# Kernel tuning notes

Hardware: AMD Instinct MI355X
Metric: run time of the kernel (lower is better)

## Reference

```python
import jax, jax.numpy as jnp
from jax import lax
import numpy as np

B, T, C_IN, H, W = 2, 4, 128, 64, 64
D_MODEL, N_Q, N_POINTS, PATCH, N_LAYERS = 256, 300, 8, 3, 6


def _sine_pos(Hh, Ww, d, temperature=10000.0):
    # mask is all-False, so cumsum of ones -> arange(1..H)/H * 2pi
    two_pi = 2.0 * np.pi
    yn = (jnp.arange(1, Hh + 1, dtype=jnp.float32) / (Hh + 1e-6)) * two_pi
    xn = (jnp.arange(1, Ww + 1, dtype=jnp.float32) / (Ww + 1e-6)) * two_pi
    q = d // 4
    i = jnp.arange(q, dtype=jnp.float32)
    dim_t = temperature ** (2.0 * jnp.floor(i / 2.0) / q)
    py = yn[:, None] / dim_t
    px = xn[:, None] / dim_t
    py = jnp.stack([jnp.sin(py), jnp.cos(py)], axis=-1).reshape(Hh, 2 * q)
    px = jnp.stack([jnp.sin(px), jnp.cos(px)], axis=-1).reshape(Ww, 2 * q)
    pos = jnp.concatenate([
        jnp.broadcast_to(py[:, None, :], (Hh, Ww, 2 * q)),
        jnp.broadcast_to(px[None, :, :], (Hh, Ww, 2 * q)),
    ], axis=-1)
    return jnp.transpose(pos, (2, 0, 1))  # [d,H,W]


def _sample_scale(fmap, ref, ps):
    # fmap [B,C,h,w]; ref [B,nQ,nP,2] in [0,1]. Bilinear grid_sample,
    # padding_mode='border', align_corners=True -> direct gather (no replication).
    Bc, C, h, w = fmap.shape
    half = (ps - 1) / 2.0
    off = jnp.linspace(-half, half, ps, dtype=jnp.float32)
    oy, ox = jnp.meshgrid(off, off, indexing='ij')  # [ps,ps]
    gx = ref[..., 0, None, None] * 2.0 - 1.0 + ox * (2.0 / w)  # [B,nQ,nP,ps,ps]
    gy = ref[..., 1, None, None] * 2.0 - 1.0 + oy * (2.0 / h)
    x = jnp.clip((gx + 1.0) * 0.5 * (w - 1), 0.0, w - 1.0)
    y = jnp.clip((gy + 1.0) * 0.5 * (h - 1), 0.0, h - 1.0)
    x0 = jnp.floor(x); y0 = jnp.floor(y)
    wx = x - x0; wy = y - y0
    x0i = x0.astype(jnp.int32); y0i = y0.astype(jnp.int32)
    x1i = jnp.minimum(x0i + 1, w - 1); y1i = jnp.minimum(y0i + 1, h - 1)

    def per_b(fb, y0b, x0b, y1b, x1b, wxb, wyb):
        v00 = fb[:, y0b, x0b]  # [C,nQ,nP,ps,ps]
        v01 = fb[:, y0b, x1b]
        v10 = fb[:, y1b, x0b]
        v11 = fb[:, y1b, x1b]
        return (v00 * (1 - wxb) * (1 - wyb) + v01 * wxb * (1 - wyb)
                + v10 * (1 - wxb) * wyb + v11 * wxb * wyb)

    out = jax.vmap(per_b)(fmap, y0i, x0i, y1i, x1i, wx, wy)  # [B,C,nQ,nP,ps,ps]
    return jnp.transpose(out, (0, 2, 3, 4, 5, 1))  # [B,nQ,nP,ps,ps,C]


def reference(feat, pred_boxes_init, w_tf, b_tf, w_in, b_in, w_lat, b_lat, w_sm, b_sm,
              q_embed, q_pos, Wq, bq, Wo, bo, Wp1, bp1, Wp2, bp2,
              w_r1, b_r1, w_r2, b_r2, w_b1, b_b1, w_b2, b_b2, w_cls, b_cls):
    Bb, Tt, Cin, Hh, Ww = feat.shape
    d = w_in.shape[0]
    nP = w_r2.shape[0] // 2
    ps = int(round((Wp1.shape[-1] // d) ** 0.5))
    # temporal fuse: Conv3d kernel (3,1,1), padding (1,0,0)
    x = lax.conv_general_dilated(jnp.transpose(feat, (0, 2, 1, 3, 4)), w_tf,
                                 (1, 1, 1), [(1, 1), (0, 0), (0, 0)],
                                 dimension_numbers=('NCDHW', 'OIDHW', 'NCDHW'))
    x = x + b_tf[None, :, None, None, None]
    x = x.mean(axis=2)  # [B,Cin,H,W]
    x = jnp.einsum('bchw,dc->bdhw', x, w_in) + b_in[None, :, None, None]
    x = x + _sine_pos(Hh, Ww, d)[None]
    # FPN over scales {1,2,4}: avg_pool -> 1x1 lateral -> 3x3 smooth
    feats = []
    for i, s in enumerate((1, 2, 4)):
        xi = x if s == 1 else x.reshape(Bb, d, Hh // s, s, Ww // s, s).mean(axis=(3, 5))
        xi = jnp.einsum('bchw,oc->bohw', xi, w_lat[i]) + b_lat[i][None, :, None, None]
        xi = lax.conv_general_dilated(xi, w_sm[i], (1, 1), [(1, 1), (1, 1)],
                                      dimension_numbers=('NCHW', 'OIHW', 'NCHW'))
        xi = xi + b_sm[i][None, :, None, None]
        feats.append(xi)
    nQ = q_embed.shape[0]
    queries = jnp.broadcast_to((q_embed + q_pos)[None], (Bb, nQ, d))
    boxes = pred_boxes_init
    inv_sqrt_d = 1.0 / float(np.sqrt(d))
    for l in range(Wq.shape[0]):
        h1 = jax.nn.relu(jnp.einsum('bqd,od->bqo', queries, w_r1) + b_r1)
        ro = jnp.tanh(jnp.einsum('bqd,od->bqo', h1, w_r2) + b_r2)
        ro = ro.reshape(Bb, nQ, nP, 2) * 0.5
        ref = jnp.clip(boxes[:, :, None, :2] + ro, 0.0, 1.0)
        sampled = jnp.concatenate([_sample_scale(f, ref, ps) for f in feats], axis=2)
        sampled = sampled[:, :, :nP]  # truncate multi-scale concat back to nP
        flat = sampled.reshape(Bb, nQ, nP, ps * ps * d)
        pv = jax.nn.relu(jnp.einsum('bqpi,oi->bqpo', flat, Wp1[l]) + bp1[l])
        pv = jnp.einsum('bqpd,od->bqpo', pv, Wp2[l]) + bp2[l]
        kv = pv.mean(axis=2)  # [B,nP_q,d] -> [B,nQ,d]
        q = jnp.einsum('bqd,od->bqo', queries, Wq[l]) + bq[l]
        attn = jax.nn.softmax(jnp.einsum('bqd,bkd->bqk', q, kv) * inv_sqrt_d, axis=-1)
        out = jnp.einsum('bqk,bkd->bqd', attn, kv)
        queries = queries + (jnp.einsum('bqd,od->bqo', out, Wo[l]) + bo[l])
        hb = jax.nn.relu(jnp.einsum('bqd,od->bqo', queries, w_b1) + b_b1)
        delta = jax.nn.sigmoid(jnp.einsum('bqd,od->bqo', hb, w_b2) + b_b2)
        boxes = jnp.clip(boxes + 0.1 * jnp.tanh(delta - 0.5), 0.0, 1.0)
    logits = (jnp.einsum('bqd,od->bqo', queries, w_cls) + b_cls)[..., 0]
    return logits, boxes


def setup_inputs() -> dict:
    key = jax.random.key(0)
    keys = iter(jax.random.split(key, 48))

    def nrm(shape, s=0.02):
        return jax.random.normal(next(keys), shape, dtype=jnp.float32) * s

    inp = {
        'feat': jax.random.normal(next(keys), (B, T, C_IN, H, W), dtype=jnp.float32),
        'pred_boxes_init': jax.random.uniform(next(keys), (B, N_Q, 4), dtype=jnp.float32),
        'w_tf': nrm((C_IN, C_IN, 3, 1, 1)), 'b_tf': jnp.zeros((C_IN,), jnp.float32),
        'w_in': nrm((D_MODEL, C_IN)), 'b_in': jnp.zeros((D_MODEL,), jnp.float32),
        'w_lat': nrm((3, D_MODEL, D_MODEL)), 'b_lat': jnp.zeros((3, D_MODEL), jnp.float32),
        'w_sm': nrm((3, D_MODEL, D_MODEL, 3, 3)), 'b_sm': jnp.zeros((3, D_MODEL), jnp.float32),
        'q_embed': nrm((N_Q, D_MODEL), 1.0), 'q_pos': nrm((N_Q, D_MODEL), 1.0),
        'Wq': nrm((N_LAYERS, D_MODEL, D_MODEL)), 'bq': jnp.zeros((N_LAYERS, D_MODEL), jnp.float32),
        'Wo': nrm((N_LAYERS, D_MODEL, D_MODEL)), 'bo': jnp.zeros((N_LAYERS, D_MODEL), jnp.float32),
        'Wp1': nrm((N_LAYERS, D_MODEL, PATCH * PATCH * D_MODEL)), 'bp1': jnp.zeros((N_LAYERS, D_MODEL), jnp.float32),
        'Wp2': nrm((N_LAYERS, D_MODEL, D_MODEL)), 'bp2': jnp.zeros((N_LAYERS, D_MODEL), jnp.float32),
        'w_r1': nrm((D_MODEL, D_MODEL)), 'b_r1': jnp.zeros((D_MODEL,), jnp.float32),
        'w_r2': nrm((2 * N_POINTS, D_MODEL)), 'b_r2': jnp.zeros((2 * N_POINTS,), jnp.float32),
        'w_b1': nrm((D_MODEL, D_MODEL)), 'b_b1': jnp.zeros((D_MODEL,), jnp.float32),
        'w_b2': nrm((4, D_MODEL)), 'b_b2': jnp.zeros((4,), jnp.float32),
        'w_cls': nrm((1, D_MODEL)), 'b_cls': jnp.zeros((1,), jnp.float32),
    }
    return inp
```

## Files before the change

kernel.cpp:

```cpp
#include <hip/hip_runtime.h>
#include <hip/hip_bf16.h>
#include <math.h>

#define BB 2
#define TT 4
#define CIN 128
#define DM 256
#define NQ 300
#define NP 8
#define PS 3
#define NL 6
#define HW 4096
#define KP 2304

typedef __attribute__((ext_vector_type(8))) short short8;
typedef __attribute__((ext_vector_type(4))) short short4_t;
typedef __attribute__((ext_vector_type(4))) float f32x4;
typedef unsigned short ushort_t;

static __device__ __forceinline__ ushort_t f2bf(float f) {
  __hip_bfloat16 h = __float2bfloat16(f);
  return *reinterpret_cast<ushort_t*>(&h);
}
static __device__ __forceinline__ float bf2f(ushort_t u) {
// ... 119 lines not shown
    }
    if (btr) {
      const float* sp = Bsrc + (size_t)(k0 + oo) * 256 + bn + mg;
      float4 f0 = *(const float4*)sp;
      float4 f1 = *(const float4*)(sp + 4);
      ushort_t* dst = Bs + oo;
      dst[(mg + 0) * 36] = f2bf(f0.x); dst[(mg + 1) * 36] = f2bf(f0.y);
      dst[(mg + 2) * 36] = f2bf(f0.z); dst[(mg + 3) * 36] = f2bf(f0.w);
      dst[(mg + 4) * 36] = f2bf(f1.x); dst[(mg + 5) * 36] = f2bf(f1.y);
      dst[(mg + 6) * 36] = f2bf(f1.z); dst[(mg + 7) * 36] = f2bf(f1.w);
    } else {
      const float* sp = Bsrc + (size_t)(bn + nr) * 256 + k0 + kg;
      float4 f0 = *(const float4*)sp;
      float4 f1 = *(const float4*)(sp + 4);
      short8 v;
      v[0] = (short)f2bf(f0.x); v[1] = (short)f2bf(f0.y);
      v[2] = (short)f2bf(f0.z); v[3] = (short)f2bf(f0.w);
      v[4] = (short)f2bf(f1.x); v[5] = (short)f2bf(f1.y);
      v[6] = (short)f2bf(f1.z); v[7] = (short)f2bf(f1.w);
      *(short8*)(Bs + nr * 36 + kg) = v;
    }
    __syncthreads();
    short8 a0 = *(const short8*)(As + (wm + ml) * 36 + q * 8);
    short8 a1 = *(const short8*)(As + (wm + 16 + ml) * 36 + q * 8);
    short8 b0 = *(const short8*)(Bs + (wn + ml) * 36 + q * 8);
    short8 b1 = *(const short8*)(Bs + (wn + 16 + ml) * 36 + q * 8);
    acc[0][0] = __builtin_amdgcn_mfma_f32_16x16x32_bf16(a0, b0, acc[0][0], 0, 0, 0);
    acc[0][1] = __builtin_amdgcn_mfma_f32_16x16x32_bf16(a0, b1, acc[0][1], 0, 0, 0);
    acc[1][0] = __builtin_amdgcn_mfma_f32_16x16x32_bf16(a1, b0, acc[1][0], 0, 0, 0);
    acc[1][1] = __builtin_amdgcn_mfma_f32_16x16x32_bf16(a1, b1, acc[1][1], 0, 0, 0);
    __syncthreads();
  }
#pragma unroll
  for (int i = 0; i < 2; ++i)
#pragma unroll
    for (int j = 0; j < 2; ++j) {
      int cn = bn + wn + j * 16 + ml;
#pragma unroll
      for (int r = 0; r < 4; ++r) {
        int rm = bm + wm + i * 16 + q * 4 + r;
        C[(size_t)rm * 256 + cn] = f2bf(acc[i][j][r]);
      }
    }
}

__global__ __launch_bounds__(256) void k_tr(const float* __restrict__ feat,
                                            ushort_t* __restrict__ featT) {
  __shared__ float ldsF[64][65];
  int tid = threadIdx.x;
  int gs = blockIdx.x;
  int b = gs >> 6;
  int s0 = (gs & 63) * 64;
  int k0 = blockIdx.y * 64;
  int kk = tid >> 2, sc0 = (tid & 3) * 16;
  {
    int k = k0 + kk;
    int u = k >> 7, ci = k & 127;
    const float* src = feat + (((size_t)(b * 4 + u) * 128 + ci) << 12) + s0 + sc0;
#pragma unroll
    for (int j = 0; j < 4; ++j) {
      float4 v = *(const float4*)(src + j * 4);
      ldsF[kk][sc0 + j * 4 + 0] = v.x;
      ldsF[kk][sc0 + j * 4 + 1] = v.y;
      ldsF[kk][sc0 + j * 4 + 2] = v.z;
      ldsF[kk][sc0 + j * 4 + 3] = v.w;
    }
  }
  __syncthreads();
#pragma unroll
  for (int p = 0; p < 2; ++p) {
    int idx = p * 256 + tid;
    int s_l = idx >> 3, kc = (idx & 7) * 8;
    short8 v;
#pragma unroll
    for (int j = 0; j < 8; ++j) v[j] = (short)f2bf(ldsF[kc + j][s_l]);
    *(short8*)(featT + (size_t)(b * 4096 + s0 + s_l) * 512 + k0 + kc) = v;
  }
}

__global__ __launch_bounds__(256) void k_feat2(const ushort_t* __restrict__ featT,
                                               const ushort_t* __restrict__ wcomb,
                                               const float* __restrict__ biasc,
                                               ushort_t* __restrict__ xcl) {
  __shared__ ushort_t As[32 * 36];
  __shared__ ushort_t Bs[64 * 36];
  __shared__ float dimt_s[256];
  int tid = threadIdx.x;
  {
    int dd = tid & 127;
    int ii = dd >> 1;
    dimt_s[tid] = powf(10000.0f, (2.0f * (float)(ii >> 1)) / 64.0f);
  }
  int bm = blockIdx.x * 32, bn = blockIdx.y * 64;
  int w = tid >> 6, lane = tid & 63;
  int wm = (w & 1) * 16, wn = (w >> 1) * 32;
  int q = lane >> 4, ml = lane & 15;
  int sra = tid >> 3, sca = (tid & 7) * 4;
  int srb = tid >> 2, scb = (tid & 3) * 8;
  const ushort_t* Ag = featT + (size_t)(bm + sra) * 512 + sca;
  const ushort_t* Wg = wcomb + (size_t)(bn + srb) * 512 + scb;
  f32x4 acc[2] = {};
  short4_t av = *(const short4_t*)Ag;
  short8 wv = *(const short8*)Wg;
  for (int k0 = 0; k0 < 512; k0 += 32) {
    *(short4_t*)(As + sra * 36 + sca) = av;
    *(short8*)(Bs + srb * 36 + scb) = wv;
    __syncthreads();
    if (k0 + 32 < 512) {
      av = *(const short4_t*)(Ag + k0 + 32);
      wv = *(const short8*)(Wg + k0 + 32);
    }
    short8 a = *(const short8*)(As + (wm + ml) * 36 + q * 8);
    short8 b0 = *(const short8*)(Bs + (wn + ml) * 36 + q * 8);
    short8 b1 = *(const short8*)(Bs + (wn + 16 + ml) * 36 + q * 8);
    acc[0] = __builtin_amdgcn_mfma_f32_16x16x32_bf16(a, b0, acc[0], 0, 0, 0);
    acc[1] = __builtin_amdgcn_mfma_f32_16x16x32_bf16(a, b1, acc[1], 0, 0, 0);
    __syncthreads();
  }
  const float FKT = 6.28318530717958647692f / 64.000001f;
#pragma unroll
  for (int j = 0; j < 2; ++j) {
    int cn = bn + wn + j * 16 + ml;
    float dimt = dimt_s[cn];
    float bC = biasc[cn];
    bool isx = cn >= 128;
    bool isc = cn & 1;
#pragma unroll
    for (int r = 0; r < 4; ++r) {
      int rm = bm + wm + q * 4 + r;
      int s = rm & 4095;
      int y = s >> 6, x = s & 63;
      float ang = (float)((isx ? x : y) + 1) * FKT / dimt;
      float pos = isc ? cosf(ang) : sinf(ang);
      xcl[(size_t)rm * 256 + cn] = f2bf(acc[j][r] + bC + pos);
    }
  }
}

template <int ACT, int OUTMODE, int MG>
__global__ __launch_bounds__(256) void k_gemm_bf16(const ushort_t* __restrict__ A,
                                                   const ushort_t* __restrict__ W,
                                                   const float* __restrict__ bias,
                                                   const float* __restrict__ res,
                                                   float* __restrict__ Cf,
                                                   ushort_t* __restrict__ Cb,
                                                   int M, int N, int K,
                                                   const ushort_t* __restrict__ W2,
                                                   const float* __restrict__ bias2,
                                                   const ushort_t* __restrict__ W3,
                                                   const float* __restrict__ bias3) {
  __shared__ ushort_t As[64 * 36];
  __shared__ ushort_t Bs[64 * 36];
  int tid = threadIdx.x;
  int bm = blockIdx.x * 64, bn = blockIdx.y * 64;
  int w = tid >> 6, lane = tid & 63;
  int wm = (w & 1) * 32, wn = (w >> 1) * 32;
  int q = lane >> 4, ml = lane & 15;
  f32x4 acc[2][2] = {};
  int srow = tid >> 2, scol = (tid & 3) * 8;
  int ga = bm + srow;
  if (MG) ga = min(ga, M - 1);
  const ushort_t* Ag = A + (size_t)ga * K + scol;
  const ushort_t* Wg;
  if (OUTMODE == 7) {
    int seg = bn >> 8;
    const ushort_t* Wb = (seg == 0) ? W : ((seg == 1) ? W2 : W3);
    Wg = Wb + (size_t)((bn & 255) + srow) * K + scol;
  } else if (OUTMODE == 4) {
    const ushort_t* Wb = (bn < 256) ? W : W2;
    Wg = Wb + (size_t)((bn & 255) + srow) * K + scol;
  } else {
    Wg = W + (size_t)(bn + srow) * K + scol;
  }
  short8 av = *(const short8*)(Ag);
  short8 wv = *(const short8*)(Wg);
  for (int k0 = 0; k0 < K; k0 += 32) {
    *(short8*)(As + srow * 36 + scol) = av;
    *(short8*)(Bs + srow * 36 + scol) = wv;
    __syncthreads();
    if (k0 + 32 < K) {
      av = *(const short8*)(Ag + k0 + 32);
      wv = *(const short8*)(Wg + k0 + 32);
    }
    short8 a0 = *(const short8*)(As + (wm + ml) * 36 + q * 8);
    short8 a1 = *(const short8*)(As + (wm + 16 + ml) * 36 + q * 8);
    short8 b0 = *(const short8*)(Bs + (wn + ml) * 36 + q * 8);
    short8 b1 = *(const short8*)(Bs + (wn + 16 + ml) * 36 + q * 8);
    acc[0][0] = __builtin_amdgcn_mfma_f32_16x16x32_bf16(a0, b0, acc[0][0], 0, 0, 0);
    acc[0][1] = __builtin_amdgcn_mfma_f32_16x16x32_bf16(a0, b1, acc[0][1], 0, 0, 0);
    acc[1][0] = __builtin_amdgcn_mfma_f32_16x16x32_bf16(a1, b0, acc[1][0], 0, 0, 0);
    acc[1][1] = __builtin_amdgcn_mfma_f32_16x16x32_bf16(a1, b1, acc[1][1], 0, 0, 0);
    __syncthreads();
  }
#pragma unroll
  for (int i = 0; i < 2; ++i) {
#pragma unroll
    for (int j = 0; j < 2; ++j) {
      int cn = bn + wn + j * 16 + ml;
      float bsv;
      if (OUTMODE == 7) {
        int seg = cn >> 8;
        bsv = ((seg == 0) ? bias : ((seg == 1) ? bias2 : bias3))[cn & 255];
      } else if (OUTMODE == 4) {
        bsv = ((cn < 256) ? bias : bias2)[cn & 255];
      } else {
        bsv = bias ? bias[cn] : 0.f;
      }
#pragma unroll
      for (int r = 0; r < 4; ++r) {
        int rm = bm + wm + i * 16 + q * 4 + r;
        if (MG && rm >= M) continue;
        float v = acc[i][j][r] + bsv;
        if (OUTMODE == 0) {
          if (ACT == 1) v = fmaxf(v, 0.f);
          Cf[(size_t)rm * N + cn] = v;
        } else if (OUTMODE == 1) {
          int b = rm >> 12, rem = rm & 4095;
          int y = rem >> 6, xx = rem & 63;
          Cb[(((size_t)(b * 66 + y + 1)) * 66 + xx + 1) * 256 + cn] = f2bf(v);
        } else if (OUTMODE == 4) {
          if (cn < 256) Cf[(size_t)rm * 256 + cn] = fmaxf(v, 0.f);
          else Cb[(size_t)rm * 256 + (cn & 255)] = f2bf(v);
        } else if (OUTMODE == 6) {
          Cb[(size_t)rm * N + cn] = f2bf(v);
        } else if (OUTMODE == 7) {
          if (cn < 256) Cf[(size_t)rm * 256 + cn] = fmaxf(v, 0.f);
          else if (cn < 512) ((float*)Cb)[(size_t)rm * 256 + (cn & 255)] = fmaxf(v, 0.f);
          else ((ushort_t*)res)[(size_t)rm * 256 + (cn & 255)] = f2bf(v);
        }
      }
    }
  }
}

__global__ __launch_bounds__(256) void k_wp1_split(const ushort_t* __restrict__ A,
                                                   const ushort_t* __restrict__ W,
                                                   ushort_t* __restrict__ part) {
  __shared__ ushort_t As[64 * 36];
  __shared__ ushort_t Bs[64 * 36];
  int tid = threadIdx.x;
  int bm = blockIdx.x * 64, bn = blockIdx.y * 64;
  int kz = blockIdx.z * 768;
  int w = tid >> 6, lane = tid & 63;
  int wm = (w & 1) * 32, wn = (w >> 1) * 32;
  int q = lane >> 4, ml = lane & 15;
  int srow = tid >> 2, scol = (tid & 3) * 8;
  const ushort_t* Ag = A + (size_t)(bm + srow) * KP + kz + scol;
  const ushort_t* Wg = W + (size_t)(bn + srow) * KP + kz + scol;
  f32x4 acc[2][2] = {};
  short8 av = *(const short8*)(Ag);
  short8 wv = *(const short8*)(Wg);
  for (int k0 = 0; k0 < 768; k0 += 32) {
    *(short8*)(As + srow * 36 + scol) = av;
    *(short8*)(Bs + srow * 36 + scol) = wv;
    __syncthreads();
    if (k0 + 32 < 768) {
      av = *(const short8*)(Ag + k0 + 32);
      wv = *(const short8*)(Wg + k0 + 32);
    }
    short8 a0 = *(const short8*)(As + (wm + ml) * 36 + q * 8);
    short8 a1 = *(const short8*)(As + (wm + 16 + ml) * 36 + q * 8);
    short8 b0 = *(const short8*)(Bs + (wn + ml) * 36 + q * 8);
    short8 b1 = *(const short8*)(Bs + (wn + 16 + ml) * 36 + q * 8);
    acc[0][0] = __builtin_amdgcn_mfma_f32_16x16x32_bf16(a0, b0, acc[0][0], 0, 0, 0);
    acc[0][1] = __builtin_amdgcn_mfma_f32_16x16x32_bf16(a0, b1, acc[0][1], 0, 0, 0);
    acc[1][0] = __builtin_amdgcn_mfma_f32_16x16x32_bf16(a1, b0, acc[1][0], 0, 0, 0);
    acc[1][1] = __builtin_amdgcn_mfma_f32_16x16x32_bf16(a1, b1, acc[1][1], 0, 0, 0);
    __syncthreads();
  }
  ushort_t* pz = part + (size_t)blockIdx.z * 4800 * 256;
#pragma unroll
  for (int i = 0; i < 2; ++i)
#pragma unroll
    for (int j = 0; j < 2; ++j) {
      int cn = bn + wn + j * 16 + ml;
#pragma unroll
      for (int r = 0; r < 4; ++r) {
        int rm = bm + wm + i * 16 + q * 4 + r;
        pz[(size_t)rm * 256 + cn] = f2bf(acc[i][j][r]);
      }
    }
}

__global__ __launch_bounds__(256) void k_wp1_reduce(const ushort_t* __restrict__ part,
                                                    const float* __restrict__ bias,
                                                    ushort_t* __restrict__ pvm) {
  int row = blockIdx.x;
  int d = threadIdx.x;
  float b = bias[d];
  float s = 0.f;
#pragma unroll
  for (int p = 0; p < 8; ++p) {
    size_t idx = (size_t)(row * 8 + p) * 256 + d;
    float v = bf2f(part[idx]) + bf2f(part[idx + (size_t)4800 * 256]) +
              bf2f(part[idx + (size_t)2 * 4800 * 256]) + b;
    s += fmaxf(v, 0.f);
  }
  pvm[(size_t)row * 256 + d] = f2bf(s * 0.125f);
}

__global__ __launch_bounds__(256) void k_conv3(const ushort_t* __restrict__ x2p,
                                               const ushort_t* __restrict__ wsm,
                                               const float* __restrict__ bsm,
                                               ushort_t* __restrict__ fcl) {
  __shared__ ushort_t As[32 * 36];
  __shared__ ushort_t Bs[64 * 36];
  int tid = threadIdx.x;
  int bm = blockIdx.x * 32, bn = blockIdx.y * 64;
  int w = tid >> 6, lane = tid & 63;
  int wm = (w & 1) * 16, wn = (w >> 1) * 32;
  int q = lane >> 4, ml = lane & 15;
  int sra = tid >> 3, sca = (tid & 7) * 4;
  int srb = tid >> 2, scb = (tid & 3) * 8;
  int sA = bm + sra;
  int b = sA >> 12, rem = sA & 4095;
  size_t pbase = ((size_t)(b * 66 + (rem >> 6)) * 66 + (rem & 63)) * 256;
  const ushort_t* Wg = wsm + (size_t)(bn + srb) * KP + scb;
  auto loadA = [&](int k0) {
    int ka = k0 + sca;
    int t9 = ka >> 8;
    int ky = t9 / 3, kx = t9 - ky * 3;
    return *(const short4_t*)(x2p + pbase + (size_t)(ky * 66 + kx) * 256 + (ka & 255));
  };
  f32x4 acc[2] = {};
  short4_t av = loadA(0);
  short8 wv = *(const short8*)(Wg);
  for (int k0 = 0; k0 < KP; k0 += 32) {
    *(short4_t*)(As + sra * 36 + sca) = av;
    *(short8*)(Bs + srb * 36 + scb) = wv;
    __syncthreads();
    if (k0 + 32 < KP) {
      av = loadA(k0 + 32);
      wv = *(const short8*)(Wg + k0 + 32);
    }
    short8 a = *(const short8*)(As + (wm + ml) * 36 + q * 8);
    short8 b0 = *(const short8*)(Bs + (wn + ml) * 36 + q * 8);
    short8 b1 = *(const short8*)(Bs + (wn + 16 + ml) * 36 + q * 8);
    acc[0] = __builtin_amdgcn_mfma_f32_16x16x32_bf16(a, b0, acc[0], 0, 0, 0);
    acc[1] = __builtin_amdgcn_mfma_f32_16x16x32_bf16(a, b1, acc[1], 0, 0, 0);
    __syncthreads();
  }
#pragma unroll
  for (int j = 0; j < 2; ++j) {
    int cn = bn + wn + j * 16 + ml;
    float bsv = bsm[cn];
#pragma unroll
    for (int r = 0; r < 4; ++r) {
      int rm = bm + wm + q * 4 + r;
      fcl[(size_t)rm * 256 + cn] = f2bf(acc[j][r] + bsv);
    }
  }
}

__global__ __launch_bounds__(256) void k_sample(const ushort_t* __restrict__ fcl,
                                                const float* __restrict__ h1,
                                                const float* __restrict__ w_r2,
                                                const float* __restrict__ b_r2,
                                                const float* __restrict__ boxesIn,
                                                float* __restrict__ boxesOut,
                                                const float* __restrict__ hb,
                                                const float* __restrict__ w_b2,
                                                const float* __restrict__ b_b2,
                                                ushort_t* __restrict__ flat) {
  __shared__ float pr[8];
  __shared__ float bc2[2];
  __shared__ float nb2[2];
  int blk = blockIdx.x;
  int row = blk >> 3, p = blk & 7;
  int b = row / NQ;
  int tid = threadIdx.x;
  int w = tid >> 6, lane = tid & 63;
  if (hb) {
    float4 hv = *(const float4*)(hb + (size_t)row * 256 + lane * 4);
    float4 wv = *(const float4*)(w_b2 + (size_t)w * 256 + lane * 4);
    float aa = hv.x * wv.x + hv.y * wv.y + hv.z * wv.z + hv.w * wv.w;
#pragma unroll
    for (int s = 32; s > 0; s >>= 1) aa += __shfl_down(aa, s, 64);
    if (lane == 0) {
      aa += b_b2[w];
      float delta = 1.0f / (1.0f + expf(-aa));
      float v = boxesIn[row * 4 + w] + 0.1f * tanhf(delta - 0.5f);
      v = fminf(fmaxf(v, 0.f), 1.f);
      if (w < 2) nb2[w] = v;
      if (p == 0) boxesOut[row * 4 + w] = v;
    }
  } else if (tid < 2) {
    nb2[tid] = boxesIn[row * 4 + tid];
  }
  float h = h1[(size_t)row * 256 + tid];
  float px = h * w_r2[(size_t)(2 * p) * 256 + tid];
  float py = h * w_r2[(size_t)(2 * p + 1) * 256 + tid];
#pragma unroll
  for (int s = 32; s > 0; s >>= 1) {
    px += __shfl_down(px, s, 64);
    py += __shfl_down(py, s, 64);
  }
  if (lane == 0) { pr[w * 2] = px; pr[w * 2 + 1] = py; }
  __syncthreads();
  if (tid == 0) {
    float sx = pr[0] + pr[2] + pr[4] + pr[6] + b_r2[2 * p];
    float sy = pr[1] + pr[3] + pr[5] + pr[7] + b_r2[2 * p + 1];
    float rx = nb2[0] + 0.5f * tanhf(sx);
    float ry = nb2[1] + 0.5f * tanhf(sy);
    bc2[0] = fminf(fmaxf(rx, 0.f), 1.f);
    bc2[1] = fminf(fmaxf(ry, 0.f), 1.f);
  }
  __syncthreads();
  float rx = bc2[0], ry = bc2[1];
  int c = tid;
  const ushort_t* fb = fcl + (size_t)b * HW * DM;
  ushort_t* op = flat + (size_t)blk * KP;
#pragma unroll
  for (int jy = 0; jy < 3; ++jy) {
    float yy = (ry + (float)(jy - 1) * (1.0f / 64.0f)) * 63.0f;
    yy = fminf(fmaxf(yy, 0.f), 63.0f);
    float y0f = floorf(yy);
    float wy = yy - y0f;
    int y0 = (int)y0f;
    int y1 = min(y0 + 1, 63);
#pragma unroll
    for (int jx = 0; jx < 3; ++jx) {
      float xx = (rx + (float)(jx - 1) * (1.0f / 64.0f)) * 63.0f;
      xx = fminf(fmaxf(xx, 0.f), 63.0f);
      float x0f = floorf(xx);
      float wx = xx - x0f;
      int x0 = (int)x0f;
      int x1 = min(x0 + 1, 63);
      float v00 = bf2f(fb[(y0 * 64 + x0) * DM + c]);
      float v01 = bf2f(fb[(y0 * 64 + x1) * DM + c]);
      float v10 = bf2f(fb[(y1 * 64 + x0) * DM + c]);
      float v11 = bf2f(fb[(y1 * 64 + x1) * DM + c]);
      float v = v00 * (1.f - wx) * (1.f - wy) + v01 * wx * (1.f - wy) +
                v10 * (1.f - wx) * wy + v11 * wx * wy;
      op[(jy * 3 + jx) * DM + c] = f2bf(v);
    }
  }
}

__global__ __launch_bounds__(256) void k_attn(const ushort_t* __restrict__ qt,
                                              const ushort_t* __restrict__ pvm,
                                              const ushort_t* __restrict__ wfT,
                                              const float* __restrict__ bfuse_l,
                                              float* __restrict__ queries,
                                              ushort_t* __restrict__ qbf) {
  __shared__ float qs[256];
  __shared__ float sc[512];
  __shared__ float red[256];
  __shared__ float pr4[1024];
  int row = blockIdx.x;
  int b = row / NQ;
  int tid = threadIdx.x;
  qs[tid] = bf2f(qt[(size_t)row * DM + tid]);
  __syncthreads();
  const ushort_t* kvB = pvm + (size_t)b * NQ * DM;
#pragma unroll
  for (int s2 = 0; s2 < 2; ++s2) {
    int k = tid + s2 * 256;
    float v = -1e30f;
    if (k < NQ) {
      const ushort_t* kp = kvB + (size_t)k * DM;
      float a = 0.f;
#pragma unroll
      for (int d = 0; d < 256; d += 8) {
        short8 k8 = *(const short8*)(kp + d);
        const float* qd = qs + d;
        a += bf2f((ushort_t)k8[0]) * qd[0];
        a += bf2f((ushort_t)k8[1]) * qd[1];
        a += bf2f((ushort_t)k8[2]) * qd[2];
        a += bf2f((ushort_t)k8[3]) * qd[3];
        a += bf2f((ushort_t)k8[4]) * qd[4];
        a += bf2f((ushort_t)k8[5]) * qd[5];
        a += bf2f((ushort_t)k8[6]) * qd[6];
        a += bf2f((ushort_t)k8[7]) * qd[7];
      }
      v = a * (1.0f / 16.0f);
    }
    sc[k] = v;
  }
  __syncthreads();
  red[tid] = fmaxf(sc[tid], sc[tid + 256]);
  __syncthreads();
  for (int st = 128; st > 0; st >>= 1) {
    if (tid < st) red[tid] = fmaxf(red[tid], red[tid + st]);
    __syncthreads();
  }
  float mx = red[0];
  __syncthreads();
  float e0 = (tid < NQ) ? expf(sc[tid] - mx) : 0.f;
  float e1 = (tid + 256 < NQ) ? expf(sc[tid + 256] - mx) : 0.f;
  sc[tid] = e0;
  sc[tid + 256] = e1;
  red[tid] = e0 + e1;
  __syncthreads();
  for (int st = 128; st > 0; st >>= 1) {
    if (tid < st) red[tid] += red[tid + st];
    __syncthreads();
  }
  float inv = 1.0f / red[0];
  __syncthreads();
  float acc = 0.f;
#pragma unroll 4
  for (int k = 0; k < NQ; ++k)
    acc += sc[k] * bf2f(kvB[(size_t)k * DM + tid]);
  qs[tid] = acc * inv;
  __syncthreads();
  int oq = (tid & 63) * 4, dq = (tid >> 6) * 64;
  float a0 = 0.f, a1 = 0.f, a2 = 0.f, a3 = 0.f;
  const ushort_t* wp = wfT + (size_t)dq * 256 + oq;
#pragma unroll 8
  for (int dd = 0; dd < 64; ++dd) {
    float cc = qs[dq + dd];
    short4_t wv = *(const short4_t*)(wp + (size_t)dd * 256);
    a0 += cc * bf2f((ushort_t)wv[0]);
    a1 += cc * bf2f((ushort_t)wv[1]);
    a2 += cc * bf2f((ushort_t)wv[2]);
    a3 += cc * bf2f((ushort_t)wv[3]);
  }
// ... 46 lines not shown
    }
  }
}

extern "C" void kernel_launch(void* const* d_in, const int* in_sizes, int n_in,
                              void* d_out, int out_size, void* d_ws, size_t ws_size,
                              hipStream_t stream) {
  const float* feat   = (const float*)d_in[0];
  const float* pb     = (const float*)d_in[1];
  const float* w_tf   = (const float*)d_in[2];
  const float* b_tf   = (const float*)d_in[3];
  const float* w_in   = (const float*)d_in[4];
  const float* b_in   = (const float*)d_in[5];
  const float* w_lat  = (const float*)d_in[6];
  const float* b_lat  = (const float*)d_in[7];
  const float* w_sm   = (const float*)d_in[8];
  const float* b_sm   = (const float*)d_in[9];
  const float* q_embed= (const float*)d_in[10];
  const float* q_pos  = (const float*)d_in[11];
  const float* Wq     = (const float*)d_in[12];
  const float* bq     = (const float*)d_in[13];
  const float* Wo     = (const float*)d_in[14];
  const float* bo     = (const float*)d_in[15];
  const float* Wp1    = (const float*)d_in[16];
  const float* bp1    = (const float*)d_in[17];
  const float* Wp2    = (const float*)d_in[18];
  const float* bp2    = (const float*)d_in[19];
  const float* w_r1   = (const float*)d_in[20];
  const float* b_r1   = (const float*)d_in[21];
  const float* w_r2   = (const float*)d_in[22];
  const float* b_r2   = (const float*)d_in[23];
  const float* w_b1   = (const float*)d_in[24];
  const float* b_b1   = (const float*)d_in[25];
  const float* w_b2   = (const float*)d_in[26];
  const float* b_b2   = (const float*)d_in[27];
  const float* w_cls  = (const float*)d_in[28];
  const float* b_cls  = (const float*)d_in[29];
  float* out = (float*)d_out;

  float* ws = (float*)d_ws;
  size_t off = 0;
  auto alloc = [&](size_t n) { float* p = ws + off; off += n; return p; };
  ushort_t* flat    = (ushort_t*)alloc(5529600);
  ushort_t* part    = (ushort_t*)alloc(1843200);
  ushort_t* featT   = (ushort_t*)alloc(2097152);
  ushort_t* xcl     = (ushort_t*)alloc(1048576);
  ushort_t* x2p     = (ushort_t*)alloc(1115136);
  ushort_t* fcl     = (ushort_t*)alloc(1048576);
  ushort_t* wcomb   = (ushort_t*)alloc(65536);
  ushort_t* tct     = (ushort_t*)alloc(32768);
  ushort_t* win_bf  = (ushort_t*)alloc(16384);
  float*    biasc   = alloc(256);
  ushort_t* wlat_bf = (ushort_t*)alloc(32768);
  ushort_t* wsm_bf  = (ushort_t*)alloc(294912);
  ushort_t* wp1_bf  = (ushort_t*)alloc(1769472);
  ushort_t* wb1_bf  = (ushort_t*)alloc(32768);
  ushort_t* wr1_bf  = (ushort_t*)alloc(32768);
  ushort_t* wqt_bf  = (ushort_t*)alloc(196608);
  ushort_t* wfuseT  = (ushort_t*)alloc(196608);
  float*    bqt     = alloc(1536);
  float*    bfuse   = alloc(1536);
  float* queries = alloc(153600);
  ushort_t* qbf  = (ushort_t*)alloc(76800);
  float* h1      = alloc(153600);
  ushort_t* qt   = (ushort_t*)alloc(76800);
  float* hb      = alloc(153600);
  ushort_t* pvm  = (ushort_t*)alloc(76800);
  float* boxesA  = alloc(2400);
  float* boxesB  = alloc(2400);
  (void)ws_size; (void)in_sizes; (void)n_in; (void)out_size;

  k_prep<<<7942, 256, 0, stream>>>(w_in, w_lat, w_b1, w_r1, Wp1,
                                   win_bf, wlat_bf, wb1_bf, wr1_bf, wp1_bf,
                                   w_tf, tct, w_sm, wsm_bf,
                                   Wp2, Wo, bq, bp2, bo, bqt, bfuse,
                                   (uint4*)x2p, b_tf, b_in, biasc,
                                   q_embed, q_pos, pb, queries, qbf, boxesA);
  k_gemm_bf16<0, 6, 0><<<dim3(4, 8), 256, 0, stream>>>(win_bf, tct, nullptr, nullptr,
                                                       nullptr, wcomb, 256, 512, 128,
                                                       nullptr, nullptr, nullptr, nullptr);
  k_wcompose<<<dim3(4, 4, 12), 256, 0, stream>>>(Wp2, Wq, Wo, wqt_bf, wfuseT);

  k_tr<<<dim3(128, 8), 256, 0, stream>>>(feat, featT);
  k_feat2<<<dim3(256, 4), 256, 0, stream>>>(featT, wcomb, biasc, xcl);
  k_gemm_bf16<0, 1, 0><<<dim3(128, 4), 256, 0, stream>>>(xcl, wlat_bf, b_lat, nullptr,
                                                         nullptr, x2p, BB * HW, 256, 256,
                                                         nullptr, nullptr, nullptr, nullptr);
  k_conv3<<<dim3(256, 4), 256, 0, stream>>>(x2p, wsm_bf, b_sm, fcl);

  const int M6 = BB * NQ;
  const int Mp = BB * NQ * NP;
  dim3 g600w((M6 + 63) / 64, 8);
  dim3 g600m((M6 + 63) / 64, 12);
  dim3 gsk(Mp / 64, 4, 3);

  k_gemm_bf16<0, 4, 1><<<g600w, 256, 0, stream>>>(qbf, wr1_bf, b_r1, nullptr, h1,
                                                  qt, M6, 512, 256,
                                                  wqt_bf, bqt, nullptr, nullptr);
  float* bcur = boxesA;
  float* bnext = boxesB;
  for (int l = 0; l < NL; ++l) {
    const float* hbp = (l == 0) ? nullptr : hb;
    k_sample<<<Mp, 256, 0, stream>>>(fcl, h1, w_r2, b_r2, bcur, bnext,
                                     hbp, w_b2, b_b2, flat);
    if (l > 0) { float* tmp = bcur; bcur = bnext; bnext = tmp; }
    k_wp1_split<<<gsk, 256, 0, stream>>>(flat, wp1_bf + (size_t)l * 256 * KP, part);
    k_wp1_reduce<<<600, 256, 0, stream>>>(part, bp1 + (size_t)l * DM, pvm);
    k_attn<<<M6, 256, 0, stream>>>(qt, pvm, wfuseT + (size_t)l * 65536,
                                   bfuse + l * 256, queries, qbf);
    int ln = (l + 1) % NL;
    k_gemm_bf16<0, 7, 1><<<g600m, 256, 0, stream>>>(qbf, wb1_bf, b_b1, (const float*)qt,
                                                    hb, (ushort_t*)h1, M6, 768, 256,
                                                    wr1_bf, b_r1,
                                                    wqt_bf + (size_t)ln * 65536,
                                                    bqt + ln * 256);
  }
  k_boxf<<<M6, 256, 0, stream>>>(hb, w_b2, b_b2, bcur, 1,
                                 queries, w_cls, b_cls, out);
}
```

Before: 697.2 us.

## Enlarge GEMM tiles in feat2/conv3/wp1 and restructure sampling per query row

The feature-projection and 3x3 conv GEMMs now use 64x64 tiles with a 2x2 MFMA block per wave instead of 32x64. The Wp1 split-K GEMM uses 128x64 tiles with eight MFMAs per wave and bounds checks on the ragged tail. k_sample now runs one 512-thread block per query that computes all 8 point offsets once, instead of one block per point that repeated the box update and offset reductions. Each change cuts redundant loads and launch count in exchange for fewer blocks and less parallelism on the GPU.

```diff
diff --git a/kernel.cpp b/kernel.cpp
--- a/kernel.cpp
+++ b/kernel.cpp
@@ -225,7 +225,7 @@
                                                const ushort_t* __restrict__ wcomb,
                                                const float* __restrict__ biasc,
                                                ushort_t* __restrict__ xcl) {
-  __shared__ ushort_t As[32 * 36];
+  __shared__ ushort_t As[64 * 36];
   __shared__ ushort_t Bs[64 * 36];
   __shared__ float dimt_s[256];
   int tid = threadIdx.x;
@@ -234,50 +234,54 @@
     int ii = dd >> 1;
     dimt_s[tid] = powf(10000.0f, (2.0f * (float)(ii >> 1)) / 64.0f);
   }
-  int bm = blockIdx.x * 32, bn = blockIdx.y * 64;
+  int bm = blockIdx.x * 64, bn = blockIdx.y * 64;
   int w = tid >> 6, lane = tid & 63;
-  int wm = (w & 1) * 16, wn = (w >> 1) * 32;
+  int wm = (w & 1) * 32, wn = (w >> 1) * 32;
   int q = lane >> 4, ml = lane & 15;
-  int sra = tid >> 3, sca = (tid & 7) * 4;
-  int srb = tid >> 2, scb = (tid & 3) * 8;
-  const ushort_t* Ag = featT + (size_t)(bm + sra) * 512 + sca;
-  const ushort_t* Wg = wcomb + (size_t)(bn + srb) * 512 + scb;
-  f32x4 acc[2] = {};
-  short4_t av = *(const short4_t*)Ag;
+  int srow = tid >> 2, scol = (tid & 3) * 8;
+  const ushort_t* Ag = featT + (size_t)(bm + srow) * 512 + scol;
+  const ushort_t* Wg = wcomb + (size_t)(bn + srow) * 512 + scol;
+  f32x4 acc[2][2] = {};
+  short8 av = *(const short8*)Ag;
   short8 wv = *(const short8*)Wg;
   for (int k0 = 0; k0 < 512; k0 += 32) {
-    *(short4_t*)(As + sra * 36 + sca) = av;
-    *(short8*)(Bs + srb * 36 + scb) = wv;
+    *(short8*)(As + srow * 36 + scol) = av;
+    *(short8*)(Bs + srow * 36 + scol) = wv;
     __syncthreads();
     if (k0 + 32 < 512) {
-      av = *(const short4_t*)(Ag + k0 + 32);
+      av = *(const short8*)(Ag + k0 + 32);
       wv = *(const short8*)(Wg + k0 + 32);
     }
-    short8 a = *(const short8*)(As + (wm + ml) * 36 + q * 8);
+    short8 a0 = *(const short8*)(As + (wm + ml) * 36 + q * 8);
+    short8 a1 = *(const short8*)(As + (wm + 16 + ml) * 36 + q * 8);
     short8 b0 = *(const short8*)(Bs + (wn + ml) * 36 + q * 8);
     short8 b1 = *(const short8*)(Bs + (wn + 16 + ml) * 36 + q * 8);
-    acc[0] = __builtin_amdgcn_mfma_f32_16x16x32_bf16(a, b0, acc[0], 0, 0, 0);
-    acc[1] = __builtin_amdgcn_mfma_f32_16x16x32_bf16(a, b1, acc[1], 0, 0, 0);
+    acc[0][0] = __builtin_amdgcn_mfma_f32_16x16x32_bf16(a0, b0, acc[0][0], 0, 0, 0);
+    acc[0][1] = __builtin_amdgcn_mfma_f32_16x16x32_bf16(a0, b1, acc[0][1], 0, 0, 0);
+    acc[1][0] = __builtin_amdgcn_mfma_f32_16x16x32_bf16(a1, b0, acc[1][0], 0, 0, 0);
+    acc[1][1] = __builtin_amdgcn_mfma_f32_16x16x32_bf16(a1, b1, acc[1][1], 0, 0, 0);
     __syncthreads();
   }
   const float FKT = 6.28318530717958647692f / 64.000001f;
 #pragma unroll
-  for (int j = 0; j < 2; ++j) {
-    int cn = bn + wn + j * 16 + ml;
-    float dimt = dimt_s[cn];
-    float bC = biasc[cn];
-    bool isx = cn >= 128;
-    bool isc = cn & 1;
-#pragma unroll
-    for (int r = 0; r < 4; ++r) {
-      int rm = bm + wm + q * 4 + r;
-      int s = rm & 4095;
-      int y = s >> 6, x = s & 63;
-      float ang = (float)((isx ? x : y) + 1) * FKT / dimt;
-      float pos = isc ? cosf(ang) : sinf(ang);
-      xcl[(size_t)rm * 256 + cn] = f2bf(acc[j][r] + bC + pos);
-    }
-  }
+  for (int i = 0; i < 2; ++i)
+#pragma unroll
+    for (int j = 0; j < 2; ++j) {
+      int cn = bn + wn + j * 16 + ml;
+      float dimt = dimt_s[cn];
+      float bC = biasc[cn];
+      bool isx = cn >= 128;
+      bool isc = cn & 1;
+#pragma unroll
+      for (int r = 0; r < 4; ++r) {
+        int rm = bm + wm + i * 16 + q * 4 + r;
+        int s = rm & 4095;
+        int y = s >> 6, x = s & 63;
+        float ang = (float)((isx ? x : y) + 1) * FKT / dimt;
+        float pos = isc ? cosf(ang) : sinf(ang);
+        xcl[(size_t)rm * 256 + cn] = f2bf(acc[i][j][r] + bC + pos);
+      }
+    }
 }
 
 template <int ACT, int OUTMODE, int MG>
@@ -379,26 +383,111 @@
 __global__ __launch_bounds__(256) void k_wp1_split(const ushort_t* __restrict__ A,
                                                    const ushort_t* __restrict__ W,
                                                    ushort_t* __restrict__ part) {
+  __shared__ ushort_t As[128 * 36];
+  __shared__ ushort_t Bs[64 * 36];
+  int tid = threadIdx.x;
+  int bm = blockIdx.x * 128, bn = blockIdx.y * 64;
+  int kz = blockIdx.z * 768;
+  int w = tid >> 6, lane = tid & 63;
+  int wm = w * 32;
+  int q = lane >> 4, ml = lane & 15;
+  int srA = tid >> 1, scA = (tid & 1) * 16;
+  int srB = tid >> 2, scB = (tid & 3) * 8;
+  int ga = min(bm + srA, 4800 - 1);
+  const ushort_t* Ag = A + (size_t)ga * KP + kz + scA;
+  const ushort_t* Wg = W + (size_t)(bn + srB) * KP + kz + scB;
+  f32x4 acc[2][4] = {};
+  short8 av0 = *(const short8*)(Ag);
+  short8 av1 = *(const short8*)(Ag + 8);
+  short8 wv = *(const short8*)(Wg);
+  for (int k0 = 0; k0 < 768; k0 += 32) {
+    *(short8*)(As + srA * 36 + scA) = av0;
+    *(short8*)(As + srA * 36 + scA + 8) = av1;
+    *(short8*)(Bs + srB * 36 + scB) = wv;
+    __syncthreads();
+    if (k0 + 32 < 768) {
+      av0 = *(const short8*)(Ag + k0 + 32);
+      av1 = *(const short8*)(Ag + k0 + 40);
+      wv = *(const short8*)(Wg + k0 + 32);
+    }
+    short8 a0 = *(const short8*)(As + (wm + ml) * 36 + q * 8);
+    short8 a1 = *(const short8*)(As + (wm + 16 + ml) * 36 + q * 8);
+    short8 b0 = *(const short8*)(Bs + (ml) * 36 + q * 8);
+    short8 b1 = *(const short8*)(Bs + (16 + ml) * 36 + q * 8);
+    short8 b2 = *(const short8*)(Bs + (32 + ml) * 36 + q * 8);
+    short8 b3 = *(const short8*)(Bs + (48 + ml) * 36 + q * 8);
+    acc[0][0] = __builtin_amdgcn_mfma_f32_16x16x32_bf16(a0, b0, acc[0][0], 0, 0, 0);
+    acc[0][1] = __builtin_amdgcn_mfma_f32_16x16x32_bf16(a0, b1, acc[0][1], 0, 0, 0);
+    acc[0][2] = __builtin_amdgcn_mfma_f32_16x16x32_bf16(a0, b2, acc[0][2], 0, 0, 0);
+    acc[0][3] = __builtin_amdgcn_mfma_f32_16x16x32_bf16(a0, b3, acc[0][3], 0, 0, 0);
+    acc[1][0] = __builtin_amdgcn_mfma_f32_16x16x32_bf16(a1, b0, acc[1][0], 0, 0, 0);
+    acc[1][1] = __builtin_amdgcn_mfma_f32_16x16x32_bf16(a1, b1, acc[1][1], 0, 0, 0);
+    acc[1][2] = __builtin_amdgcn_mfma_f32_16x16x32_bf16(a1, b2, acc[1][2], 0, 0, 0);
+    acc[1][3] = __builtin_amdgcn_mfma_f32_16x16x32_bf16(a1, b3, acc[1][3], 0, 0, 0);
+    __syncthreads();
+  }
+  ushort_t* pz = part + (size_t)blockIdx.z * 4800 * 256;
+#pragma unroll
+  for (int i = 0; i < 2; ++i)
+#pragma unroll
+    for (int j = 0; j < 4; ++j) {
+      int cn = bn + j * 16 + ml;
+#pragma unroll
+      for (int r = 0; r < 4; ++r) {
+        int rm = bm + wm + i * 16 + q * 4 + r;
+        if (rm < 4800) pz[(size_t)rm * 256 + cn] = f2bf(acc[i][j][r]);
+      }
+    }
+}
+
+__global__ __launch_bounds__(256) void k_wp1_reduce(const ushort_t* __restrict__ part,
+                                                    const float* __restrict__ bias,
+                                                    ushort_t* __restrict__ pvm) {
+  int row = blockIdx.x;
+  int d = threadIdx.x;
+  float b = bias[d];
+  float s = 0.f;
+#pragma unroll
+  for (int p = 0; p < 8; ++p) {
+    size_t idx = (size_t)(row * 8 + p) * 256 + d;
+    float v = bf2f(part[idx]) + bf2f(part[idx + (size_t)4800 * 256]) +
+              bf2f(part[idx + (size_t)2 * 4800 * 256]) + b;
+    s += fmaxf(v, 0.f);
+  }
+  pvm[(size_t)row * 256 + d] = f2bf(s * 0.125f);
+}
+
+__global__ __launch_bounds__(256) void k_conv3(const ushort_t* __restrict__ x2p,
+                                               const ushort_t* __restrict__ wsm,
+                                               const float* __restrict__ bsm,
+                                               ushort_t* __restrict__ fcl) {
   __shared__ ushort_t As[64 * 36];
   __shared__ ushort_t Bs[64 * 36];
   int tid = threadIdx.x;
   int bm = blockIdx.x * 64, bn = blockIdx.y * 64;
-  int kz = blockIdx.z * 768;
   int w = tid >> 6, lane = tid & 63;
   int wm = (w & 1) * 32, wn = (w >> 1) * 32;
   int q = lane >> 4, ml = lane & 15;
   int srow = tid >> 2, scol = (tid & 3) * 8;
-  const ushort_t* Ag = A + (size_t)(bm + srow) * KP + kz + scol;
-  const ushort_t* Wg = W + (size_t)(bn + srow) * KP + kz + scol;
+  int sA = bm + srow;
+  int b = sA >> 12, rem = sA & 4095;
+  size_t pbase = ((size_t)(b * 66 + (rem >> 6)) * 66 + (rem & 63)) * 256;
+  const ushort_t* Wg = wsm + (size_t)(bn + srow) * KP + scol;
+  auto loadA = [&](int k0) {
+    int ka = k0 + scol;
+    int t9 = ka >> 8;
+    int ky = t9 / 3, kx = t9 - ky * 3;
+    return *(const short8*)(x2p + pbase + (size_t)(ky * 66 + kx) * 256 + (ka & 255));
+  };
   f32x4 acc[2][2] = {};
-  short8 av = *(const short8*)(Ag);
+  short8 av = loadA(0);
   short8 wv = *(const short8*)(Wg);
-  for (int k0 = 0; k0 < 768; k0 += 32) {
+  for (int k0 = 0; k0 < KP; k0 += 32) {
     *(short8*)(As + srow * 36 + scol) = av;
     *(short8*)(Bs + srow * 36 + scol) = wv;
     __syncthreads();
-    if (k0 + 32 < 768) {
-      av = *(const short8*)(Ag + k0 + 32);
+    if (k0 + 32 < KP) {
+      av = loadA(k0 + 32);
       wv = *(const short8*)(Wg + k0 + 32);
     }
     short8 a0 = *(const short8*)(As + (wm + ml) * 36 + q * 8);
@@ -411,91 +500,21 @@
     acc[1][1] = __builtin_amdgcn_mfma_f32_16x16x32_bf16(a1, b1, acc[1][1], 0, 0, 0);
     __syncthreads();
   }
-  ushort_t* pz = part + (size_t)blockIdx.z * 4800 * 256;
 #pragma unroll
   for (int i = 0; i < 2; ++i)
 #pragma unroll
     for (int j = 0; j < 2; ++j) {
       int cn = bn + wn + j * 16 + ml;
+      float bsv = bsm[cn];
 #pragma unroll
       for (int r = 0; r < 4; ++r) {
         int rm = bm + wm + i * 16 + q * 4 + r;
-        pz[(size_t)rm * 256 + cn] = f2bf(acc[i][j][r]);
+        fcl[(size_t)rm * 256 + cn] = f2bf(acc[i][j][r] + bsv);
       }
     }
 }
 
-__global__ __launch_bounds__(256) void k_wp1_reduce(const ushort_t* __restrict__ part,
-                                                    const float* __restrict__ bias,
-                                                    ushort_t* __restrict__ pvm) {
-  int row = blockIdx.x;
-  int d = threadIdx.x;
-  float b = bias[d];
-  float s = 0.f;
-#pragma unroll
-  for (int p = 0; p < 8; ++p) {
-    size_t idx = (size_t)(row * 8 + p) * 256 + d;
-    float v = bf2f(part[idx]) + bf2f(part[idx + (size_t)4800 * 256]) +
-              bf2f(part[idx + (size_t)2 * 4800 * 256]) + b;
-    s += fmaxf(v, 0.f);
-  }
-  pvm[(size_t)row * 256 + d] = f2bf(s * 0.125f);
-}
-
-__global__ __launch_bounds__(256) void k_conv3(const ushort_t* __restrict__ x2p,
-                                               const ushort_t* __restrict__ wsm,
-                                               const float* __restrict__ bsm,
-                                               ushort_t* __restrict__ fcl) {
-  __shared__ ushort_t As[32 * 36];
-  __shared__ ushort_t Bs[64 * 36];
-  int tid = threadIdx.x;
-  int bm = blockIdx.x * 32, bn = blockIdx.y * 64;
-  int w = tid >> 6, lane = tid & 63;
-  int wm = (w & 1) * 16, wn = (w >> 1) * 32;
-  int q = lane >> 4, ml = lane & 15;
-  int sra = tid >> 3, sca = (tid & 7) * 4;
-  int srb = tid >> 2, scb = (tid & 3) * 8;
-  int sA = bm + sra;
-  int b = sA >> 12, rem = sA & 4095;
-  size_t pbase = ((size_t)(b * 66 + (rem >> 6)) * 66 + (rem & 63)) * 256;
-  const ushort_t* Wg = wsm + (size_t)(bn + srb) * KP + scb;
-  auto loadA = [&](int k0) {
-    int ka = k0 + sca;
-    int t9 = ka >> 8;
-    int ky = t9 / 3, kx = t9 - ky * 3;
-    return *(const short4_t*)(x2p + pbase + (size_t)(ky * 66 + kx) * 256 + (ka & 255));
-  };
-  f32x4 acc[2] = {};
-  short4_t av = loadA(0);
-  short8 wv = *(const short8*)(Wg);
-  for (int k0 = 0; k0 < KP; k0 += 32) {
-    *(short4_t*)(As + sra * 36 + sca) = av;
-    *(short8*)(Bs + srb * 36 + scb) = wv;
-    __syncthreads();
-    if (k0 + 32 < KP) {
-      av = loadA(k0 + 32);
-      wv = *(const short8*)(Wg + k0 + 32);
-    }
-    short8 a = *(const short8*)(As + (wm + ml) * 36 + q * 8);
-    short8 b0 = *(const short8*)(Bs + (wn + ml) * 36 + q * 8);
-    short8 b1 = *(const short8*)(Bs + (wn + 16 + ml) * 36 + q * 8);
-    acc[0] = __builtin_amdgcn_mfma_f32_16x16x32_bf16(a, b0, acc[0], 0, 0, 0);
-    acc[1] = __builtin_amdgcn_mfma_f32_16x16x32_bf16(a, b1, acc[1], 0, 0, 0);
-    __syncthreads();
-  }
-#pragma unroll
-  for (int j = 0; j < 2; ++j) {
-    int cn = bn + wn + j * 16 + ml;
-    float bsv = bsm[cn];
-#pragma unroll
-    for (int r = 0; r < 4; ++r) {
-      int rm = bm + wm + q * 4 + r;
-      fcl[(size_t)rm * 256 + cn] = f2bf(acc[j][r] + bsv);
-    }
-  }
-}
-
-__global__ __launch_bounds__(256) void k_sample(const ushort_t* __restrict__ fcl,
+__global__ __launch_bounds__(512) void k_sample(const ushort_t* __restrict__ fcl,
                                                 const float* __restrict__ h1,
                                                 const float* __restrict__ w_r2,
                                                 const float* __restrict__ b_r2,
@@ -505,77 +524,86 @@
                                                 const float* __restrict__ w_b2,
                                                 const float* __restrict__ b_b2,
                                                 ushort_t* __restrict__ flat) {
-  __shared__ float pr[8];
-  __shared__ float bc2[2];
+  __shared__ float pr[16];
+  __shared__ float cc[8][2];
   __shared__ float nb2[2];
-  int blk = blockIdx.x;
-  int row = blk >> 3, p = blk & 7;
+  int row = blockIdx.x;
   int b = row / NQ;
   int tid = threadIdx.x;
   int w = tid >> 6, lane = tid & 63;
   if (hb) {
-    float4 hv = *(const float4*)(hb + (size_t)row * 256 + lane * 4);
-    float4 wv = *(const float4*)(w_b2 + (size_t)w * 256 + lane * 4);
-    float aa = hv.x * wv.x + hv.y * wv.y + hv.z * wv.z + hv.w * wv.w;
-#pragma unroll
-    for (int s = 32; s > 0; s >>= 1) aa += __shfl_down(aa, s, 64);
-    if (lane == 0) {
-      aa += b_b2[w];
-      float delta = 1.0f / (1.0f + expf(-aa));
-      float v = boxesIn[row * 4 + w] + 0.1f * tanhf(delta - 0.5f);
-      v = fminf(fmaxf(v, 0.f), 1.f);
-      if (w < 2) nb2[w] = v;
-      if (p == 0) boxesOut[row * 4 + w] = v;
+    if (w < 4) {
+      float4 hv = *(const float4*)(hb + (size_t)row * 256 + lane * 4);
+      float4 wv = *(const float4*)(w_b2 + (size_t)w * 256 + lane * 4);
+      float aa = hv.x * wv.x + hv.y * wv.y + hv.z * wv.z + hv.w * wv.w;
+#pragma unroll
+      for (int s = 32; s > 0; s >>= 1) aa += __shfl_down(aa, s, 64);
+      if (lane == 0) {
+        aa += b_b2[w];
+        float delta = 1.0f / (1.0f + expf(-aa));
+        float v = boxesIn[row * 4 + w] + 0.1f * tanhf(delta - 0.5f);
+        v = fminf(fmaxf(v, 0.f), 1.f);
+        boxesOut[row * 4 + w] = v;
+        if (w < 2) nb2[w] = v;
+      }
     }
   } else if (tid < 2) {
     nb2[tid] = boxesIn[row * 4 + tid];
   }
-  float h = h1[(size_t)row * 256 + tid];
-  float px = h * w_r2[(size_t)(2 * p) * 256 + tid];
-  float py = h * w_r2[(size_t)(2 * p + 1) * 256 + tid];
-#pragma unroll
-  for (int s = 32; s > 0; s >>= 1) {
-    px += __shfl_down(px, s, 64);
-    py += __shfl_down(py, s, 64);
-  }
-  if (lane == 0) { pr[w * 2] = px; pr[w * 2 + 1] = py; }
-  __syncthreads();
-  if (tid == 0) {
-    float sx = pr[0] + pr[2] + pr[4] + pr[6] + b_r2[2 * p];
-    float sy = pr[1] + pr[3] + pr[5] + pr[7] + b_r2[2 * p + 1];
+  {
+    float4 hv4 = *(const float4*)(h1 + (size_t)row * 256 + lane * 4);
+#pragma unroll
+    for (int k = 0; k < 2; ++k) {
+      int d = w * 2 + k;
+      float4 wv4 = *(const float4*)(w_r2 + (size_t)d * 256 + lane * 4);
+      float s = hv4.x * wv4.x + hv4.y * wv4.y + hv4.z * wv4.z + hv4.w * wv4.w;
+#pragma unroll
+      for (int st = 32; st > 0; st >>= 1) s += __shfl_down(s, st, 64);
+      if (lane == 0) pr[d] = s;
+    }
+  }
+  __syncthreads();
+  if (tid < 8) {
+    int p = tid;
+    float sx = pr[2 * p] + b_r2[2 * p];
+    float sy = pr[2 * p + 1] + b_r2[2 * p + 1];
     float rx = nb2[0] + 0.5f * tanhf(sx);
     float ry = nb2[1] + 0.5f * tanhf(sy);
-    bc2[0] = fminf(fmaxf(rx, 0.f), 1.f);
-    bc2[1] = fminf(fmaxf(ry, 0.f), 1.f);
-  }
-  __syncthreads();
-  float rx = bc2[0], ry = bc2[1];
-  int c = tid;
+    cc[p][0] = fminf(fmaxf(rx, 0.f), 1.f);
+    cc[p][1] = fminf(fmaxf(ry, 0.f), 1.f);
+  }
+  __syncthreads();
+  int c = tid & 255;
+  int ph = tid >> 8;
   const ushort_t* fb = fcl + (size_t)b * HW * DM;
-  ushort_t* op = flat + (size_t)blk * KP;
-#pragma unroll
-  for (int jy = 0; jy < 3; ++jy) {
-    float yy = (ry + (float)(jy - 1) * (1.0f / 64.0f)) * 63.0f;
-    yy = fminf(fmaxf(yy, 0.f), 63.0f);
-    float y0f = floorf(yy);
-    float wy = yy - y0f;
-    int y0 = (int)y0f;
-    int y1 = min(y0 + 1, 63);
-#pragma unroll
-    for (int jx = 0; jx < 3; ++jx) {
-      float xx = (rx + (float)(jx - 1) * (1.0f / 64.0f)) * 63.0f;
-      xx = fminf(fmaxf(xx, 0.f), 63.0f);
-      float x0f = floorf(xx);
-      float wx = xx - x0f;
-      int x0 = (int)x0f;
-      int x1 = min(x0 + 1, 63);
-      float v00 = bf2f(fb[(y0 * 64 + x0) * DM + c]);
-      float v01 = bf2f(fb[(y0 * 64 + x1) * DM + c]);
-      float v10 = bf2f(fb[(y1 * 64 + x0) * DM + c]);
-      float v11 = bf2f(fb[(y1 * 64 + x1) * DM + c]);
-      float v = v00 * (1.f - wx) * (1.f - wy) + v01 * wx * (1.f - wy) +
-                v10 * (1.f - wx) * wy + v11 * wx * wy;
-      op[(jy * 3 + jx) * DM + c] = f2bf(v);
+  for (int it = 0; it < 4; ++it) {
+    int p = it * 2 + ph;
+    float rx = cc[p][0], ry = cc[p][1];
+    ushort_t* op = flat + ((size_t)row * 8 + p) * KP;
+#pragma unroll
+    for (int jy = 0; jy < 3; ++jy) {
+      float yy = (ry + (float)(jy - 1) * (1.0f / 64.0f)) * 63.0f;
+      yy = fminf(fmaxf(yy, 0.f), 63.0f);
+      float y0f = floorf(yy);
+      float wy = yy - y0f;
+      int y0 = (int)y0f;
+      int y1 = min(y0 + 1, 63);
+#pragma unroll
+      for (int jx = 0; jx < 3; ++jx) {
+        float xx = (rx + (float)(jx - 1) * (1.0f / 64.0f)) * 63.0f;
+        xx = fminf(fmaxf(xx, 0.f), 63.0f);
+        float x0f = floorf(xx);
+        float wx = xx - x0f;
+        int x0 = (int)x0f;
+        int x1 = min(x0 + 1, 63);
+        float v00 = bf2f(fb[(y0 * 64 + x0) * DM + c]);
+        float v01 = bf2f(fb[(y0 * 64 + x1) * DM + c]);
+        float v10 = bf2f(fb[(y1 * 64 + x0) * DM + c]);
+        float v11 = bf2f(fb[(y1 * 64 + x1) * DM + c]);
+        float v = v00 * (1.f - wx) * (1.f - wy) + v01 * wx * (1.f - wy) +
+                  v10 * (1.f - wx) * wy + v11 * wx * wy;
+        op[(jy * 3 + jx) * DM + c] = f2bf(v);
+      }
     }
   }
 }
@@ -788,17 +816,17 @@
   k_wcompose<<<dim3(4, 4, 12), 256, 0, stream>>>(Wp2, Wq, Wo, wqt_bf, wfuseT);
 
   k_tr<<<dim3(128, 8), 256, 0, stream>>>(feat, featT);
-  k_feat2<<<dim3(256, 4), 256, 0, stream>>>(featT, wcomb, biasc, xcl);
+  k_feat2<<<dim3(128, 4), 256, 0, stream>>>(featT, wcomb, biasc, xcl);
   k_gemm_bf16<0, 1, 0><<<dim3(128, 4), 256, 0, stream>>>(xcl, wlat_bf, b_lat, nullptr,
                                                          nullptr, x2p, BB * HW, 256, 256,
                                                          nullptr, nullptr, nullptr, nullptr);
-  k_conv3<<<dim3(256, 4), 256, 0, stream>>>(x2p, wsm_bf, b_sm, fcl);
+  k_conv3<<<dim3(128, 4), 256, 0, stream>>>(x2p, wsm_bf, b_sm, fcl);
 
   const int M6 = BB * NQ;
   const int Mp = BB * NQ * NP;
   dim3 g600w((M6 + 63) / 64, 8);
   dim3 g600m((M6 + 63) / 64, 12);
-  dim3 gsk(Mp / 64, 4, 3);
+  dim3 gsk((Mp + 127) / 128, 4, 3);
 
   k_gemm_bf16<0, 4, 1><<<g600w, 256, 0, stream>>>(qbf, wr1_bf, b_r1, nullptr, h1,
                                                   qt, M6, 512, 256,
@@ -807,7 +835,7 @@
   float* bnext = boxesB;
   for (int l = 0; l < NL; ++l) {
     const float* hbp = (l == 0) ? nullptr : hb;
-    k_sample<<<Mp, 256, 0, stream>>>(fcl, h1, w_r2, b_r2, bcur, bnext,
+    k_sample<<<M6, 512, 0, stream>>>(fcl, h1, w_r2, b_r2, bcur, bnext,
                                      hbp, w_b2, b_b2, flat);
     if (l > 0) { float* tmp = bcur; bcur = bnext; bnext = tmp; }
     k_wp1_split<<<gsk, 256, 0, stream>>>(flat, wp1_bf + (size_t)l * 256 * KP, part);
```

Result: slower. 717.4 us (+2.9%).
